# Kernel tuning notes

Hardware: AMD Instinct MI355X
Metric: run time of the kernel (lower is better)

The kernel has to match this reference:

```python
import jax, jax.numpy as jnp
import numpy as np

B, N, D = 8, 2352, 512          # N = SENT_LEN*(SENT_LEN+1) pair-grid layout
SENT_LEN, L, P = 48, 2, 512     # L = entity span length, P = number of relation pairs
NER_LABELS, RE_LABELS = 16, 32


def setup_inputs() -> dict:
    key = jax.random.key(0)
    ks = jax.random.split(key, 17)
    s = 0.02
    return {
        "inputs": jax.random.normal(ks[0], (B, N, D), jnp.float32),
        "ner": jax.random.normal(ks[1], (B, SENT_LEN, D), jnp.float32),
        "re_feat": jax.random.normal(ks[2], (P, D), jnp.float32),
        "adj": jax.random.uniform(ks[3], (B, N, N), jnp.float32),
        "W0_w": jax.random.normal(ks[4], (D, D), jnp.float32) * s,
        "W0_b": jnp.zeros((D,), jnp.float32),
        "W1_w": jax.random.normal(ks[5], (D, D), jnp.float32) * s,
        "W1_b": jnp.zeros((D,), jnp.float32),
        "out_w": jax.random.normal(ks[6], (2 * D, D), jnp.float32) * s,
        "out_b": jnp.zeros((D,), jnp.float32),
        "ner_w": jax.random.normal(ks[7], (2 * D, NER_LABELS), jnp.float32) * s,
        "ner_b": jnp.zeros((NER_LABELS,), jnp.float32),
        "re_w": jax.random.normal(ks[8], (2 * D, RE_LABELS), jnp.float32) * s,
        "re_b": jnp.zeros((RE_LABELS,), jnp.float32),
        "pair_sent": jax.random.randint(ks[9], (P,), 0, B),
        "head_start": jax.random.randint(ks[10], (P,), 0, SENT_LEN - L + 1),
        "tail_start": jax.random.randint(ks[11], (P,), 0, SENT_LEN - L + 1),
        "sent_len": SENT_LEN,
    }


def reference(inputs, ner, re_feat, adj, W0_w, W0_b, W1_w, W1_b, out_w, out_b,
              ner_w, ner_b, re_w, re_b, pair_sent, head_start, tail_start, sent_len):
    # --- GCN (use_rnn=False, dropout = identity / eval) ---
    denom = jnp.sum(adj, axis=2, keepdims=True) + 1.0      # [B, N, 1]
    x = inputs
    outs = []
    for Ww, Wb in ((W0_w, W0_b), (W1_w, W1_b)):
        Ax = jnp.einsum('bnm,bmd->bnd', adj, x)            # adj.bmm(x)
        AxW = (Ax @ Ww + Wb) + (x @ Ww + Wb)               # W(Ax) + W(x)
        g = jax.nn.relu(AxW / denom)
        outs.append(g)
        x = g
    logits = jnp.concatenate(outs, axis=-1) @ out_w + out_b  # [B, N, D]

    # --- NER head: first sent_len tokens per sentence (uniform lengths) ---
    ner_logits = jnp.concatenate([ner, logits[:, :sent_len]], axis=-1) @ ner_w + ner_b

    # --- RE head: ragged gather + average over (head span x tail span) grid ---
    offs = jnp.arange(L)
    i = head_start[:, None] + offs                         # [P, L]
    j = tail_start[:, None] + offs                         # [P, L]
    idx = (i[:, :, None] + 1) * sent_len + j[:, None, :]   # [P, L, L], get_re(l, i, j)
    pg = logits[pair_sent[:, None, None], idx]             # [P, L, L, D]
    avg = jnp.mean(pg, axis=(1, 2))                        # [P, D]
    re_logits = jnp.concatenate([re_feat, avg], axis=-1) @ re_w + re_b
    return ner_logits, re_logits
```

## Files before the change

### kernel.cpp

```cpp
#include <hip/hip_runtime.h>
#include <hip/hip_bf16.h>

#define B_    8
#define NP    2352
#define D_    512
#define SENT  48
#define PAIRS 512
#define NERL  16
#define REL   32
#define MTOT  (B_*NP)
#define SLOTB 640
#define MG    (B_*SLOTB)
#define GSCALE 32.0f

typedef unsigned short u16;
typedef unsigned char  u8;
typedef __bf16 bf16x8 __attribute__((ext_vector_type(8)));
typedef float  f32x4  __attribute__((ext_vector_type(4)));

__device__ __forceinline__ u16 f2b(float f) {
  union { float f; unsigned u; } c; c.f = f;
  unsigned u = c.u;
  u += 0x7fffu + ((u >> 16) & 1u);
  return (u16)(u >> 16);
}
__device__ __forceinline__ float b2f(u16 h) {
  union { unsigned u; float f; } c; c.u = ((unsigned)h) << 16;
  return c.f;
}
__device__ __forceinline__ u8 f2f8(float f) {
  unsigned u = __float_as_uint(f);
  u8 s = (u >> 24) & 0x80;
  float a = fabsf(f);
  if (a < 0.0009765625f) return s;
  if (a >= 448.f) return s | 0x7E;
  int e = ((u >> 23) & 0xFF) - 127;
  if (e < -6) {
    int q = (int)(a * 512.f + 0.5f);
    if (q >= 8) return s | 0x08;
    return s | (u8)q;
  }
  float sc = __uint_as_float((unsigned)((127 - e) << 23));
  int q = (int)(a * sc * 8.f + 0.5f);
  if (q >= 16) { q = 8; ++e; if (e > 8) return s | 0x7E; }
  return s | (u8)(((e + 7) << 3) | (q - 8));
}
#if defined(__has_builtin)
#if __has_builtin(__builtin_amdgcn_cvt_pk_fp8_f32)
#define HAVE_CVT_FP8 1
#endif
#endif
__device__ __forceinline__ unsigned f2f8x4(float a, float b, float c, float d) {
#ifdef HAVE_CVT_FP8
  unsigned w = 0;
  w = __builtin_amdgcn_cvt_pk_fp8_f32(a, b, w, false);
  w = __builtin_amdgcn_cvt_pk_fp8_f32(c, d, w, true);
  return w;
#else
  return (unsigned)f2f8(a) | ((unsigned)f2f8(b) << 8) |
         ((unsigned)f2f8(c) << 16) | ((unsigned)f2f8(d) << 24);
#endif
}
__device__ __forceinline__ float f82f(u8 v) {
  unsigned s = ((unsigned)(v & 0x80u)) << 24;
  unsigned e = (v >> 3) & 0xF, m = v & 7;
  if (e == 0) {
    if (m == 0) return __uint_as_float(s);
    float f = (float)m * 0.001953125f;
    return __uint_as_float(s | __float_as_uint(f));
  }
  return __uint_as_float(s | ((e + 120u) << 23) | (m << 20));
}
__device__ __forceinline__ void gload16(const void* g, void* lds) {
  __builtin_amdgcn_global_load_lds(
      (const __attribute__((address_space(1))) unsigned*)g,
      (__attribute__((address_space(3))) unsigned*)lds, 16, 0, 0);
}

template<int OUT8>
__device__ __forceinline__ void tcvt_body(const float* __restrict__ in_,
                                          void* __restrict__ out,
                                          int R, int C, int b, int r0, int c0,
                                          size_t inb, size_t outb,
                                          u16 tile[64][65]) {
  const int t  = threadIdx.x;
  const int tr = t >> 4, tc = (t & 15) * 4;
  #pragma unroll
  for (int i = 0; i < 4; ++i) {
    int rl = i * 16 + tr;
    int r  = r0 + rl;
    if (r < R) {
      const float* in = in_ + (size_t)b * inb + (size_t)r * C + c0 + tc;
      float4 v = *(const float4*)in;
      tile[rl][tc + 0] = f2b(v.x); tile[rl][tc + 1] = f2b(v.y);
      tile[rl][tc + 2] = f2b(v.z); tile[rl][tc + 3] = f2b(v.w);
    }
  }
  __syncthreads();
  const int c  = t >> 2;
  const int rb = (t & 3) * 16;
  #pragma unroll
  for (int i = 0; i < 4; ++i) {
    int rl = rb + i * 4;
    int r  = r0 + rl;
    if (OUT8) {
      u8* orow = (u8*)out + (size_t)b * outb + (size_t)(c0 + c) * R + r0;
      if (r + 3 < R) {
        *(unsigned*)(orow + rl) =
            f2f8x4(b2f(tile[rl + 0][c]), b2f(tile[rl + 1][c]),
                   b2f(tile[rl + 2][c]), b2f(tile[rl + 3][c]));
      } else {
        for (int j = 0; j < 4; ++j)
          if (r + j < R) orow[rl + j] = f2f8(b2f(tile[rl + j][c]));
      }
    } else {
      u16* orow = (u16*)out + (size_t)b * outb + (size_t)(c0 + c) * R + r0;
      if (r + 3 < R) {
        ushort4 v;
        v.x = tile[rl + 0][c]; v.y = tile[rl + 1][c];
        v.z = tile[rl + 2][c]; v.w = tile[rl + 3][c];
        *(ushort4*)(orow + rl) = v;
      } else {
        for (int j = 0; j < 4; ++j)
          if (r + j < R) orow[rl + j] = tile[rl + j][c];
      }
    }
  }
}

__global__ __launch_bounds__(256) void fat_prep(
    const float* __restrict__ adj, const float* __restrict__ inputs,
    const float* __restrict__ W0w, const float* __restrict__ W1w,
    const float* __restrict__ outw,
    const int* __restrict__ ps, const int* __restrict__ hs,
    const int* __restrict__ ts,
    u8* __restrict__ adj8, float* __restrict__ rdenom,
    u8* __restrict__ xt8, u16* __restrict__ w0t, u16* __restrict__ w1t,
    u16* __restrict__ owt, int* __restrict__ rowmap, int* __restrict__ pslot,
    u16* __restrict__ zp) {
  __shared__ u16 tile[64][65];
  __shared__ int sps[PAIRS];
  __shared__ float red[4];
  const int bx = blockIdx.x;
  const int t  = threadIdx.x;

  if (bx < MTOT) {
    const int row = bx;
    const float4* src = (const float4*)(adj + (size_t)row * NP);
    u8* dst = adj8 + (size_t)row * NP;
    float s = 0.f;
    for (int i = t; i < NP / 4; i += 256) {
      float4 v = src[i];
      s += (v.x + v.y) + (v.z + v.w);
      *(unsigned*)(dst + i * 4) = f2f8x4(v.x, v.y, v.z, v.w);
    }
    #pragma unroll
    for (int o = 32; o > 0; o >>= 1) s += __shfl_down(s, o, 64);
    int w = t >> 6, l = t & 63;
    if (l == 0) red[w] = s;
    __syncthreads();
    if (t == 0)
      rdenom[row] = 1.f / (red[0] + red[1] + red[2] + red[3] + 1.f);
  } else if (bx == MTOT) {
    zp[t] = 0; zp[256 + t] = 0;
  } else if (bx == MTOT + 1) {
    sps[t] = ps[t]; sps[256 + t] = ps[256 + t];
    for (int i = t; i < MG; i += 256) rowmap[i] = 0;
    __syncthreads();
    for (int u = t; u < B_ * SENT; u += 256)
      rowmap[(u / SENT) * SLOTB + (u % SENT)] = u % SENT;
    for (int p = t; p < PAIRS; p += 256) {
      const int b = sps[p];
      int rank = 0;
      for (int q = 0; q < p; ++q) rank += (sps[q] == b) ? 1 : 0;
      const int h = hs[p], tt = ts[p];
      const int s0 = b * SLOTB + SENT + 4 * rank;
      rowmap[s0 + 0] = (h + 1) * SENT + tt;
      rowmap[s0 + 1] = (h + 1) * SENT + tt + 1;
      rowmap[s0 + 2] = (h + 2) * SENT + tt;
      rowmap[s0 + 3] = (h + 2) * SENT + tt + 1;
      pslot[p] = s0;
    }
  } else {
    int r = bx - (MTOT + 2);
    if (r < 2368) {
      const int b = r / 296, rem = r % 296;
      const int rx = rem % 37, ry = rem / 37;
      tcvt_body<1>(inputs, xt8, NP, D_, b, rx * 64, ry * 64,
                   (size_t)NP * D_, (size_t)D_ * NP, tile);
    } else if ((r -= 2368) < 64) {
      tcvt_body<0>(W0w, w0t, 512, 512, 0, (r % 8) * 64, (r / 8) * 64,
                   0, 0, tile);
    } else if ((r -= 64) < 64) {
      tcvt_body<0>(W1w, w1t, 512, 512, 0, (r % 8) * 64, (r / 8) * 64,
                   0, 0, tile);
    } else {
      r -= 64;
      tcvt_body<0>(outw, owt, 1024, 512, 0, (r % 16) * 64, (r / 16) * 64,
                   0, 0, tile);
    }
  }
}

template<int MODE, int WRITE_T, int GATHER>
__global__ __launch_bounds__(256, 2) void gemm8(
    const void* __restrict__ A, const void* __restrict__ A2,
    const void* __restrict__ Bm, const u16* __restrict__ Xt,
    const float* __restrict__ bias, const float* __restrict__ rdenom,
    const int* __restrict__ rowmap,
    const u16* __restrict__ zp, u16* __restrict__ out, u8* __restrict__ outT,
    float ascale)
{
  constexpr bool F8   = (MODE == 0);
  constexpr int KACT   = (MODE == 0) ? NP : (MODE == 1 ? 512 : 1024);
  constexpr int KTILES = (KACT + 63) / 64;
  constexpr int EPC    = F8 ? 16 : 8;
  constexpr int CPT    = F8 ? 4 : 8;
  constexpr int NJ     = F8 ? 2 : 4;
  constexpr int ABYTES = F8 ? 8192 : 16384;

  int m0, n0, bat = 0;
  const u8* Ab = (const u8*)A;
  const u8* Bb = (const u8*)Bm;
  size_t outBase = 0;
  if constexpr (GATHER) {
    const int bx  = blockIdx.x;
    const int rid = (bx & 7) * 20 + (bx >> 3);
    const int mt  = rid >> 2;
    n0 = (rid & 3) << 7;
    m0 = mt * 128;
    bat = mt / 5;
    if constexpr (MODE == 0) {
      Ab = (const u8*)A  + (size_t)bat * NP * NP;
      Bb = (const u8*)Bm + (size_t)bat * 512 * NP;
    }
  } else if constexpr (MODE == 0) {
    const int bx  = blockIdx.x;
    bat = bx & 7;
    const int loc = bx >> 3;
    const int mt  = loc >> 2;
    n0 = (loc & 3) << 7;
    m0 = (mt < 18) ? mt * 128 : NP - 128;
    Ab = (const u8*)A  + (size_t)bat * NP * NP;
    Bb = (const u8*)Bm + (size_t)bat * 512 * NP;
    outBase = (size_t)bat * NP * 512;
  } else {
    const int bx  = blockIdx.x;
    const int xcd = bx & 7, pos = bx >> 3;
    const int rid = (xcd < 4) ? xcd * 74 + pos : 296 + (xcd - 4) * 73 + pos;
    const int mt  = rid >> 2;
    n0 = (rid & 3) << 7;
    m0 = mt * 128;
  }

  __shared__ __align__(16) u8 As[2 * ABYTES];
  __shared__ __align__(16) u8 Bs[2 * ABYTES];

  const int tid = threadIdx.x;
  const int l  = tid & 63;
  const int w  = tid >> 6;
  const int wm = w >> 1, wn = w & 1;
  const int lr = l & 15, lq = l >> 4;

  f32x4 acc[4][4];
  #pragma unroll
  for (int i = 0; i < 4; ++i)
    #pragma unroll
    for (int j = 0; j < 4; ++j)
      acc[i][j] = (f32x4){0.f, 0.f, 0.f, 0.f};

  int rsrc[2];
  #pragma unroll
  for (int j = 0; j < 2; ++j) {
    const int row = j * 64 + (tid >> 2);
    if constexpr (GATHER && MODE != 1) rsrc[j] = rowmap[m0 + row];
    else                               rsrc[j] = m0 + row;
  }

  auto STAGE = [&](int isA, int d, int kt) {
    #pragma unroll
    for (int j = 0; j < NJ; ++j) {
      const int cl   = j * 256 + tid;
      const int row  = (cl >> 2) & 127;
      const int slot = cl & 3;
      const int s    = F8 ? 0 : (cl >> 9);
      const int gch  = kt * CPT + s * 4 + (slot ^ ((row >> 1) & 3));
      const u8* src;
      if (isA) {
        if constexpr (MODE == 0) {
          src = Ab + (size_t)rsrc[j & 1] * NP + (size_t)gch * 16;
        } else if constexpr (MODE == 1) {
          src = (const u8*)A + ((size_t)(m0 + row) * 512 + (size_t)gch * 8) * 2;
        } else {
          int rg = (GATHER ? rsrc[j & 1] : (m0 + row));
          src = (gch < 64)
              ? (const u8*)A  + (((size_t)(GATHER ? bat * NP : 0) + rg) * 512
                                 + (size_t)gch * 8) * 2
              : (const u8*)A2 + ((size_t)(m0 + row) * 512
                                 + (size_t)(gch - 64) * 8) * 2;
        }
        if (gch * EPC + EPC > KACT) src = (const u8*)zp;
        gload16(src, As + d * ABYTES + cl * 16);
      } else {
        if constexpr (F8)
          src = Bb + (size_t)(n0 + row) * NP + (size_t)gch * 16;
        else
          src = (const u8*)Bm + ((size_t)(n0 + row) * KACT + (size_t)gch * 8) * 2;
        if (gch * EPC + EPC > KACT) src = (const u8*)zp;
        gload16(src, Bs + d * ABYTES + cl * 16);
      }
    }
  };

  STAGE(1, 0, 0);
  STAGE(0, 0, 0);
  asm volatile("s_waitcnt vmcnt(0)" ::: "memory");
  __builtin_amdgcn_s_barrier();

  int d = 0;
  for (int kt = 0; kt < KTILES; ++kt) {
    if (kt + 1 < KTILES) {
      STAGE(1, d ^ 1, kt + 1);
      STAGE(0, d ^ 1, kt + 1);
    }
    const u8* Ad = As + d * ABYTES;
    const u8* Bd = Bs + d * ABYTES;
    if constexpr (F8) {
      long a0[4], b0[4], a1[4], b1[4];
      #pragma unroll
      for (int f = 0; f < 4; ++f) {
        const int ra = wm * 64 + f * 16 + lr;
        const int rb = wn * 64 + f * 16 + lr;
        const int swa = (ra >> 1) & 3, swb = (rb >> 1) & 3;
        const int co = (lq >> 1), bo = (lq & 1) << 3;
        a0[f] = *(const long*)(Ad + ra * 64 + (((0 + co) ^ swa) << 4) + bo);
        b0[f] = *(const long*)(Bd + rb * 64 + (((0 + co) ^ swb) << 4) + bo);
        a1[f] = *(const long*)(Ad + ra * 64 + (((2 + co) ^ swa) << 4) + bo);
        b1[f] = *(const long*)(Bd + rb * 64 + (((2 + co) ^ swb) << 4) + bo);
      }
      asm volatile("s_waitcnt lgkmcnt(0)" ::: "memory");
      __builtin_amdgcn_sched_barrier(0);
      __builtin_amdgcn_s_setprio(1);
      #pragma unroll
      for (int mf = 0; mf < 4; ++mf)
        #pragma unroll
        for (int nf = 0; nf < 4; ++nf)
          acc[mf][nf] = __builtin_amdgcn_mfma_f32_16x16x32_fp8_fp8(
              a0[mf], b0[nf], acc[mf][nf], 0, 0, 0);
      #pragma unroll
      for (int mf = 0; mf < 4; ++mf)
        #pragma unroll
        for (int nf = 0; nf < 4; ++nf)
          acc[mf][nf] = __builtin_amdgcn_mfma_f32_16x16x32_fp8_fp8(
              a1[mf], b1[nf], acc[mf][nf], 0, 0, 0);
      __builtin_amdgcn_s_setprio(0);
      __builtin_amdgcn_sched_barrier(0);
    } else {
      bf16x8 a0[4], b0[4], a1[4], b1[4];
      #pragma unroll
      for (int f = 0; f < 4; ++f) {
        const int ra = wm * 64 + f * 16 + lr;
        const int rb = wn * 64 + f * 16 + lr;
        const int sa = (lq ^ ((ra >> 1) & 3)) << 4;
        const int sb = (lq ^ ((rb >> 1) & 3)) << 4;
        a0[f] = *(const bf16x8*)(Ad + ra * 64 + sa);
        b0[f] = *(const bf16x8*)(Bd + rb * 64 + sb);
        a1[f] = *(const bf16x8*)(Ad + 8192 + ra * 64 + sa);
        b1[f] = *(const bf16x8*)(Bd + 8192 + rb * 64 + sb);
      }
      asm volatile("s_waitcnt lgkmcnt(0)" ::: "memory");
      __builtin_amdgcn_sched_barrier(0);
      __builtin_amdgcn_s_setprio(1);
      #pragma unroll
      for (int mf = 0; mf < 4; ++mf)
        #pragma unroll
        for (int nf = 0; nf < 4; ++nf)
          acc[mf][nf] = __builtin_amdgcn_mfma_f32_16x16x32_bf16(
              a0[mf], b0[nf], acc[mf][nf], 0, 0, 0);
      #pragma unroll
      for (int mf = 0; mf < 4; ++mf)
        #pragma unroll
        for (int nf = 0; nf < 4; ++nf)
          acc[mf][nf] = __builtin_amdgcn_mfma_f32_16x16x32_bf16(
              a1[mf], b1[nf], acc[mf][nf], 0, 0, 0);
      __builtin_amdgcn_s_setprio(0);
      __builtin_amdgcn_sched_barrier(0);
    }
    asm volatile("s_waitcnt vmcnt(0)" ::: "memory");
    __builtin_amdgcn_s_barrier();
    d ^= 1;
  }

  #pragma unroll
  for (int mf = 0; mf < 4; ++mf) {
    const int gm0 = m0 + wm * 64 + mf * 16 + lq * 4;
    f32x4 rd;
    if constexpr (MODE == 1) {
      if constexpr (GATHER) {
        #pragma unroll
        for (int r = 0; r < 4; ++r)
          rd[r] = rdenom[(size_t)bat * NP + rowmap[gm0 + r]];
      } else {
        rd = *(const f32x4*)(rdenom + gm0);
      }
    }
    int rsm[4];
    if constexpr (GATHER && MODE == 0) {
      #pragma unroll
      for (int r = 0; r < 4; ++r) rsm[r] = rowmap[gm0 + r];
    }
    #pragma unroll
    for (int nf = 0; nf < 4; ++nf) {
      const int gn = n0 + wn * 64 + nf * 16 + lr;
      float vf[4];
      if constexpr (MODE == 0) {
        float xf[4];
        if constexpr (GATHER) {
          #pragma unroll
          for (int r = 0; r < 4; ++r)
            xf[r] = b2f(Xt[((size_t)bat * NP + rsm[r]) * 512 + gn]);
        } else {
          uchar4 xv = *(const uchar4*)(Bb + (size_t)gn * NP + gm0);
          xf[0] = f82f(xv.x); xf[1] = f82f(xv.y);
          xf[2] = f82f(xv.z); xf[3] = f82f(xv.w);
        }
        #pragma unroll
        for (int r = 0; r < 4; ++r) vf[r] = acc[mf][nf][r] * ascale + xf[r];
      } else if constexpr (MODE == 1) {
        const float bn = 2.f * bias[gn];
        #pragma unroll
        for (int r = 0; r < 4; ++r)
          vf[r] = fmaxf((acc[mf][nf][r] + bn) * rd[r], 0.f);
      } else {
        const float bn = bias[gn];
        #pragma unroll
        for (int r = 0; r < 4; ++r) vf[r] = acc[mf][nf][r] + bn;
      }
      #pragma unroll
      for (int r = 0; r < 4; ++r)
        out[outBase + (size_t)(gm0 + r) * 512 + gn] = f2b(vf[r]);
      if constexpr (WRITE_T) {
        const int bb = gm0 / NP;
        const int ml = gm0 - bb * NP;
        *(unsigned*)(outT + ((size_t)bb * 512 + gn) * NP + ml) =
            f2f8x4(vf[0] * GSCALE, vf[1] * GSCALE,
                   vf[2] * GSCALE, vf[3] * GSCALE);
      }
    }
  }
}

__global__ __launch_bounds__(256) void heads_kernel(
    const float* __restrict__ ner, const u16* __restrict__ logits_g,
    const float* __restrict__ nw, const float* __restrict__ nb,
    const float* __restrict__ refeat, const float* __restrict__ rw,
    const float* __restrict__ rb, const int* __restrict__ pslot,
    float* __restrict__ outp) {
  __shared__ float avg[D_];
  if (blockIdx.x < 96) {
    const int r = blockIdx.x * 4 + (threadIdx.x >> 6);
    const int b = r / SENT, tp = r % SENT;
    const int lane = threadIdx.x & 63;
    const float* nrow = ner      + ((size_t)b * SENT  + tp) * D_;
    const u16*   lrow = logits_g + ((size_t)b * SLOTB + tp) * D_;
    float rv[16];
    #pragma unroll
    for (int i = 0; i < 8; ++i) rv[i]     = nrow[lane + i * 64];
    #pragma unroll
    for (int i = 0; i < 8; ++i) rv[8 + i] = b2f(lrow[lane + i * 64]);
    for (int j = 0; j < NERL; ++j) {
      float s = 0.f;
      #pragma unroll
      for (int i = 0; i < 16; ++i)
        s = fmaf(rv[i], nw[(size_t)(lane + i * 64) * NERL + j], s);
      for (int o = 32; o > 0; o >>= 1) s += __shfl_down(s, o);
      if (lane == 0) outp[r * NERL + j] = s + nb[j];
    }
  } else {
    const int p = blockIdx.x - 96;
    const u16* r0 = logits_g + (size_t)pslot[p] * D_;
    for (int dd = threadIdx.x; dd < D_; dd += 256)
      avg[dd] = 0.25f * (b2f(r0[dd]) + b2f(r0[D_ + dd]) +
                         b2f(r0[2 * D_ + dd]) + b2f(r0[3 * D_ + dd]));
    __syncthreads();
    const int wave = threadIdx.x >> 6, lane = threadIdx.x & 63;
    const float* rf = refeat + (size_t)p * D_;
    float* out = outp + B_ * SENT * NERL;
    for (int jj = 0; jj < 8; ++jj) {
      int j = wave * 8 + jj;
      float s = 0.f;
      #pragma unroll
      for (int i = 0; i < 8; ++i) {
        int k = lane + i * 64;
        s = fmaf(rf[k],  rw[(size_t)k * REL + j], s);
        s = fmaf(avg[k], rw[(size_t)(k + D_) * REL + j], s);
      }
      for (int o = 32; o > 0; o >>= 1) s += __shfl_down(s, o);
      if (lane == 0) out[p * REL + j] = s + rb[j];
    }
  }
}

extern "C" void kernel_launch(void* const* d_in, const int* in_sizes, int n_in,
                              void* d_out, int out_size, void* d_ws, size_t ws_size,
                              hipStream_t stream) {
  const float* inputs = (const float*)d_in[0];
  const float* ner    = (const float*)d_in[1];
  const float* refeat = (const float*)d_in[2];
  const float* adj    = (const float*)d_in[3];
  const float* W0w    = (const float*)d_in[4];
  const float* W0b    = (const float*)d_in[5];
  const float* W1w    = (const float*)d_in[6];
  const float* W1b    = (const float*)d_in[7];
  const float* outw   = (const float*)d_in[8];
  const float* outb   = (const float*)d_in[9];
  const float* nerw   = (const float*)d_in[10];
  const float* nerb   = (const float*)d_in[11];
  const float* rew    = (const float*)d_in[12];
  const float* reb    = (const float*)d_in[13];
  const int*   ps     = (const int*)d_in[14];
  const int*   hs     = (const int*)d_in[15];
  const int*   ts     = (const int*)d_in[16];
  (void)in_sizes; (void)n_in; (void)out_size; (void)ws_size;
  float* outp = (float*)d_out;

  char* ws = (char*)d_ws;
  size_t off = 0;
  u8* adj8 = (u8*)(ws + off); off += (size_t)B_ * NP * NP;
  float* rdenom = (float*)(ws + off); off += (size_t)MTOT * 4;
  u16* zp  = (u16*)(ws + off); off += 1024;
  u16* w0t = (u16*)(ws + off); off += 512 * 512 * 2;
  u16* w1t = (u16*)(ws + off); off += 512 * 512 * 2;
  u16* owt = (u16*)(ws + off); off += 512 * 1024 * 2;
  u8*  xt8 = (u8*)(ws + off); off += (size_t)B_ * 512 * NP;
  u16* S   = (u16*)(ws + off); off += (size_t)MTOT * 512 * 2;
  u16* g0  = (u16*)(ws + off); off += (size_t)MTOT * 512 * 2;
  int* rowmap = (int*)(ws + off); off += (size_t)MG * 4;
  int* pslot  = (int*)(ws + off); off += (size_t)PAIRS * 4;
  u16* S_g      = (u16*)(ws + off); off += (size_t)MG * 512 * 2;
  u16* g1_g     = (u16*)(ws + off); off += (size_t)MG * 512 * 2;
  u16* logits_g = (u16*)(ws + off); off += (size_t)MG * 512 * 2;

  const int FATG = MTOT + 2 + 2368 + 64 + 64 + 128;
  fat_prep<<<FATG, 256, 0, stream>>>(adj, inputs, W0w, W1w, outw, ps, hs, ts,
                                     adj8, rdenom, xt8, w0t, w1t, owt,
                                     rowmap, pslot, zp);

  gemm8<0,0,0><<<608, 256, 0, stream>>>(adj8, nullptr, xt8, nullptr,
                                        nullptr, nullptr, nullptr, zp, S,
                                        nullptr, 1.0f);
  gemm8<1,1,0><<<588, 256, 0, stream>>>(S, nullptr, w0t, nullptr,
                                        W0b, rdenom, nullptr, zp, g0,
                                        xt8, 1.0f);
  gemm8<0,0,1><<<160, 256, 0, stream>>>(adj8, nullptr, xt8, g0,
                                        nullptr, nullptr, rowmap, zp, S_g,
                                        nullptr, 1.0f / GSCALE);
  gemm8<1,0,1><<<160, 256, 0, stream>>>(S_g, nullptr, w1t, nullptr,
                                        W1b, rdenom, rowmap, zp, g1_g,
                                        nullptr, 1.0f);
  gemm8<2,0,1><<<160, 256, 0, stream>>>(g0, g1_g, owt, nullptr,
                                        outb, nullptr, rowmap, zp, logits_g,
                                        nullptr, 1.0f);

  heads_kernel<<<608, 256, 0, stream>>>(ner, logits_g, nerw, nerb,
                                        refeat, rew, reb, pslot, outp);
}
```

Before: 284.5 us.

## Fuse adjacency fp8 conversion and row-sum into the first GEMM's A loader

This drops the separate prep pass that turned fp32 adj into an fp8 copy and computed the reciprocal degree. Both GEMMs that read adj now load the fp32 tiles into registers, convert them to fp8 and write them to LDS. The non-gather adj GEMM also accumulates row sums and writes rdenom from its n0==0 blocks. The aim is to remove the write and re-read of the 44MB fp8 adj copy and one kernel's worth of traffic. In exchange, each adj row is re-read in fp32 by four N-tile blocks, and the A path no longer uses async direct-to-LDS loads, so load latency is hidden less well.

```diff
diff --git a/kernel.cpp b/kernel.cpp
--- a/kernel.cpp
+++ b/kernel.cpp
@@ -129,41 +129,22 @@
 }
 
 __global__ __launch_bounds__(256) void fat_prep(
-    const float* __restrict__ adj, const float* __restrict__ inputs,
+    const float* __restrict__ inputs,
     const float* __restrict__ W0w, const float* __restrict__ W1w,
     const float* __restrict__ outw,
     const int* __restrict__ ps, const int* __restrict__ hs,
     const int* __restrict__ ts,
-    u8* __restrict__ adj8, float* __restrict__ rdenom,
     u8* __restrict__ xt8, u16* __restrict__ w0t, u16* __restrict__ w1t,
     u16* __restrict__ owt, int* __restrict__ rowmap, int* __restrict__ pslot,
     u16* __restrict__ zp) {
   __shared__ u16 tile[64][65];
   __shared__ int sps[PAIRS];
-  __shared__ float red[4];
   const int bx = blockIdx.x;
   const int t  = threadIdx.x;
 
-  if (bx < MTOT) {
-    const int row = bx;
-    const float4* src = (const float4*)(adj + (size_t)row * NP);
-    u8* dst = adj8 + (size_t)row * NP;
-    float s = 0.f;
-    for (int i = t; i < NP / 4; i += 256) {
-      float4 v = src[i];
-      s += (v.x + v.y) + (v.z + v.w);
-      *(unsigned*)(dst + i * 4) = f2f8x4(v.x, v.y, v.z, v.w);
-    }
-    #pragma unroll
-    for (int o = 32; o > 0; o >>= 1) s += __shfl_down(s, o, 64);
-    int w = t >> 6, l = t & 63;
-    if (l == 0) red[w] = s;
-    __syncthreads();
-    if (t == 0)
-      rdenom[row] = 1.f / (red[0] + red[1] + red[2] + red[3] + 1.f);
-  } else if (bx == MTOT) {
+  if (bx == 0) {
     zp[t] = 0; zp[256 + t] = 0;
-  } else if (bx == MTOT + 1) {
+  } else if (bx == 1) {
     sps[t] = ps[t]; sps[256 + t] = ps[256 + t];
     for (int i = t; i < MG; i += 256) rowmap[i] = 0;
     __syncthreads();
@@ -182,7 +163,7 @@
       pslot[p] = s0;
     }
   } else {
-    int r = bx - (MTOT + 2);
+    int r = bx - 2;
     if (r < 2368) {
       const int b = r / 296, rem = r % 296;
       const int rx = rem % 37, ry = rem / 37;
@@ -206,7 +187,7 @@
 __global__ __launch_bounds__(256, 2) void gemm8(
     const void* __restrict__ A, const void* __restrict__ A2,
     const void* __restrict__ Bm, const u16* __restrict__ Xt,
-    const float* __restrict__ bias, const float* __restrict__ rdenom,
+    const float* __restrict__ bias, float* __restrict__ rdenom,
     const int* __restrict__ rowmap,
     const u16* __restrict__ zp, u16* __restrict__ out, u8* __restrict__ outT,
     float ascale)
@@ -216,13 +197,13 @@
   constexpr int KTILES = (KACT + 63) / 64;
   constexpr int EPC    = F8 ? 16 : 8;
   constexpr int CPT    = F8 ? 4 : 8;
-  constexpr int NJ     = F8 ? 2 : 4;
   constexpr int ABYTES = F8 ? 8192 : 16384;
 
   int m0, n0, bat = 0;
-  const u8* Ab = (const u8*)A;
+  const float* Af = (const float*)A;
   const u8* Bb = (const u8*)Bm;
   size_t outBase = 0;
+  bool ovl = false;
   if constexpr (GATHER) {
     const int bx  = blockIdx.x;
     const int rid = (bx & 7) * 20 + (bx >> 3);
@@ -231,7 +212,7 @@
     m0 = mt * 128;
     bat = mt / 5;
     if constexpr (MODE == 0) {
-      Ab = (const u8*)A  + (size_t)bat * NP * NP;
+      Af = (const float*)A + (size_t)bat * NP * NP;
       Bb = (const u8*)Bm + (size_t)bat * 512 * NP;
     }
   } else if constexpr (MODE == 0) {
@@ -241,7 +222,8 @@
     const int mt  = loc >> 2;
     n0 = (loc & 3) << 7;
     m0 = (mt < 18) ? mt * 128 : NP - 128;
-    Ab = (const u8*)A  + (size_t)bat * NP * NP;
+    ovl = (mt == 18);
+    Af = (const float*)A + (size_t)bat * NP * NP;
     Bb = (const u8*)Bm + (size_t)bat * 512 * NP;
     outBase = (size_t)bat * NP * 512;
   } else {
@@ -277,51 +259,102 @@
     else                               rsrc[j] = m0 + row;
   }
 
-  auto STAGE = [&](int isA, int d, int kt) {
-    #pragma unroll
-    for (int j = 0; j < NJ; ++j) {
+  float4 ar[8];
+  float rsum0 = 0.f, rsum1 = 0.f;
+  auto A_LOAD = [&](int kt) {
+    #pragma unroll
+    for (int j = 0; j < 2; ++j) {
       const int cl   = j * 256 + tid;
       const int row  = (cl >> 2) & 127;
       const int slot = cl & 3;
-      const int s    = F8 ? 0 : (cl >> 9);
-      const int gch  = kt * CPT + s * 4 + (slot ^ ((row >> 1) & 3));
+      const int gch  = kt * 4 + (slot ^ ((row >> 1) & 3));
+      const float* src = Af + (size_t)rsrc[j] * NP + gch * 16;
+      if (gch * 16 + 16 > NP) src = (const float*)zp;
+      #pragma unroll
+      for (int q = 0; q < 4; ++q) ar[j * 4 + q] = *(const float4*)(src + q * 4);
+    }
+  };
+  auto A_WRITE = [&](int d) {
+    #pragma unroll
+    for (int j = 0; j < 2; ++j) {
+      const int cl = j * 256 + tid;
+      uint4 pk;
+      pk.x = f2f8x4(ar[j*4+0].x, ar[j*4+0].y, ar[j*4+0].z, ar[j*4+0].w);
+      pk.y = f2f8x4(ar[j*4+1].x, ar[j*4+1].y, ar[j*4+1].z, ar[j*4+1].w);
+      pk.z = f2f8x4(ar[j*4+2].x, ar[j*4+2].y, ar[j*4+2].z, ar[j*4+2].w);
+      pk.w = f2f8x4(ar[j*4+3].x, ar[j*4+3].y, ar[j*4+3].z, ar[j*4+3].w);
+      *(uint4*)(As + d * ABYTES + cl * 16) = pk;
+      if constexpr (MODE == 0 && !GATHER) {
+        float s = (ar[j*4+0].x + ar[j*4+0].y) + (ar[j*4+0].z + ar[j*4+0].w)
+                + (ar[j*4+1].x + ar[j*4+1].y) + (ar[j*4+1].z + ar[j*4+1].w)
+                + (ar[j*4+2].x + ar[j*4+2].y) + (ar[j*4+2].z + ar[j*4+2].w)
+                + (ar[j*4+3].x + ar[j*4+3].y) + (ar[j*4+3].z + ar[j*4+3].w);
+        if (j == 0) rsum0 += s; else rsum1 += s;
+      }
+    }
+  };
+  auto STAGE_B = [&](int d, int kt) {
+    #pragma unroll
+    for (int j = 0; j < 2; ++j) {
+      const int cl   = j * 256 + tid;
+      const int row  = (cl >> 2) & 127;
+      const int slot = cl & 3;
+      const int gch  = kt * 4 + (slot ^ ((row >> 1) & 3));
+      const u8* src  = Bb + (size_t)(n0 + row) * NP + (size_t)gch * 16;
+      if (gch * 16 + 16 > KACT) src = (const u8*)zp;
+      gload16(src, Bs + d * ABYTES + cl * 16);
+    }
+  };
+  auto STAGE_BF16 = [&](int isA, int d, int kt) {
+    #pragma unroll
+    for (int j = 0; j < 4; ++j) {
+      const int cl   = j * 256 + tid;
+      const int row  = (cl >> 2) & 127;
+      const int slot = cl & 3;
+      const int s    = cl >> 9;
+      const int gch  = kt * 8 + s * 4 + (slot ^ ((row >> 1) & 3));
       const u8* src;
       if (isA) {
-        if constexpr (MODE == 0) {
-          src = Ab + (size_t)rsrc[j & 1] * NP + (size_t)gch * 16;
-        } else if constexpr (MODE == 1) {
-          src = (const u8*)A + ((size_t)(m0 + row) * 512 + (size_t)gch * 8) * 2;
-        } else {
+        if constexpr (MODE == 2) {
           int rg = (GATHER ? rsrc[j & 1] : (m0 + row));
           src = (gch < 64)
               ? (const u8*)A  + (((size_t)(GATHER ? bat * NP : 0) + rg) * 512
                                  + (size_t)gch * 8) * 2
               : (const u8*)A2 + ((size_t)(m0 + row) * 512
                                  + (size_t)(gch - 64) * 8) * 2;
+        } else {
+          src = (const u8*)A + ((size_t)(m0 + row) * 512 + (size_t)gch * 8) * 2;
         }
         if (gch * EPC + EPC > KACT) src = (const u8*)zp;
         gload16(src, As + d * ABYTES + cl * 16);
       } else {
-        if constexpr (F8)
-          src = Bb + (size_t)(n0 + row) * NP + (size_t)gch * 16;
-        else
-          src = (const u8*)Bm + ((size_t)(n0 + row) * KACT + (size_t)gch * 8) * 2;
+        src = (const u8*)Bm + ((size_t)(n0 + row) * KACT + (size_t)gch * 8) * 2;
         if (gch * EPC + EPC > KACT) src = (const u8*)zp;
         gload16(src, Bs + d * ABYTES + cl * 16);
       }
     }
   };
 
-  STAGE(1, 0, 0);
-  STAGE(0, 0, 0);
-  asm volatile("s_waitcnt vmcnt(0)" ::: "memory");
+  if constexpr (F8) {
+    A_LOAD(0);
+    STAGE_B(0, 0);
+    asm volatile("s_waitcnt vmcnt(0)" ::: "memory");
+    A_WRITE(0);
+    asm volatile("s_waitcnt lgkmcnt(0)" ::: "memory");
+  } else {
+    STAGE_BF16(1, 0, 0);
+    STAGE_BF16(0, 0, 0);
+    asm volatile("s_waitcnt vmcnt(0)" ::: "memory");
+  }
   __builtin_amdgcn_s_barrier();
 
   int d = 0;
   for (int kt = 0; kt < KTILES; ++kt) {
-    if (kt + 1 < KTILES) {
-      STAGE(1, d ^ 1, kt + 1);
-      STAGE(0, d ^ 1, kt + 1);
+    const bool more = (kt + 1 < KTILES);
+    if constexpr (F8) {
+      if (more) { A_LOAD(kt + 1); STAGE_B(d ^ 1, kt + 1); }
+    } else {
+      if (more) { STAGE_BF16(1, d ^ 1, kt + 1); STAGE_BF16(0, d ^ 1, kt + 1); }
     }
     const u8* Ad = As + d * ABYTES;
     const u8* Bd = Bs + d * ABYTES;
@@ -355,6 +388,11 @@
               a1[mf], b1[nf], acc[mf][nf], 0, 0, 0);
       __builtin_amdgcn_s_setprio(0);
       __builtin_amdgcn_sched_barrier(0);
+      asm volatile("s_waitcnt vmcnt(0)" ::: "memory");
+      if (more) {
+        A_WRITE(d ^ 1);
+        asm volatile("s_waitcnt lgkmcnt(0)" ::: "memory");
+      }
     } else {
       bf16x8 a0[4], b0[4], a1[4], b1[4];
       #pragma unroll
@@ -385,10 +423,24 @@
               a1[mf], b1[nf], acc[mf][nf], 0, 0, 0);
       __builtin_amdgcn_s_setprio(0);
       __builtin_amdgcn_sched_barrier(0);
-    }
-    asm volatile("s_waitcnt vmcnt(0)" ::: "memory");
+      asm volatile("s_waitcnt vmcnt(0)" ::: "memory");
+    }
     __builtin_amdgcn_s_barrier();
     d ^= 1;
+  }
+
+  if constexpr (MODE == 0 && !GATHER) {
+    if (n0 == 0) {
+      #pragma unroll
+      for (int j = 0; j < 2; ++j) {
+        float s = (j == 0) ? rsum0 : rsum1;
+        s += __shfl_xor(s, 1, 64);
+        s += __shfl_xor(s, 2, 64);
+        const int lrow = j * 64 + (tid >> 2);
+        if ((l & 3) == 0 && (!ovl || m0 + lrow >= 2304))
+          rdenom[(size_t)bat * NP + m0 + lrow] = 1.f / (s + 1.f);
+      }
+    }
   }
 
   #pragma unroll
@@ -526,7 +578,6 @@
 
   char* ws = (char*)d_ws;
   size_t off = 0;
-  u8* adj8 = (u8*)(ws + off); off += (size_t)B_ * NP * NP;
   float* rdenom = (float*)(ws + off); off += (size_t)MTOT * 4;
   u16* zp  = (u16*)(ws + off); off += 1024;
   u16* w0t = (u16*)(ws + off); off += 512 * 512 * 2;
@@ -541,25 +592,24 @@
   u16* g1_g     = (u16*)(ws + off); off += (size_t)MG * 512 * 2;
   u16* logits_g = (u16*)(ws + off); off += (size_t)MG * 512 * 2;
 
-  const int FATG = MTOT + 2 + 2368 + 64 + 64 + 128;
-  fat_prep<<<FATG, 256, 0, stream>>>(adj, inputs, W0w, W1w, outw, ps, hs, ts,
-                                     adj8, rdenom, xt8, w0t, w1t, owt,
-                                     rowmap, pslot, zp);
-
-  gemm8<0,0,0><<<608, 256, 0, stream>>>(adj8, nullptr, xt8, nullptr,
-                                        nullptr, nullptr, nullptr, zp, S,
+  const int FATG = 2 + 2368 + 64 + 64 + 128;
+  fat_prep<<<FATG, 256, 0, stream>>>(inputs, W0w, W1w, outw, ps, hs, ts,
+                                     xt8, w0t, w1t, owt, rowmap, pslot, zp);
+
+  gemm8<0,0,0><<<608, 256, 0, stream>>>(adj, nullptr, xt8, nullptr,
+                                        nullptr, rdenom, nullptr, zp, S,
                                         nullptr, 1.0f);
   gemm8<1,1,0><<<588, 256, 0, stream>>>(S, nullptr, w0t, nullptr,
                                         W0b, rdenom, nullptr, zp, g0,
                                         xt8, 1.0f);
-  gemm8<0,0,1><<<160, 256, 0, stream>>>(adj8, nullptr, xt8, g0,
-                                        nullptr, nullptr, rowmap, zp, S_g,
+  gemm8<0,0,1><<<160, 256, 0, stream>>>(adj, nullptr, xt8, g0,
+                                        nullptr, rdenom, rowmap, zp, S_g,
                                         nullptr, 1.0f / GSCALE);
   gemm8<1,0,1><<<160, 256, 0, stream>>>(S_g, nullptr, w1t, nullptr,
                                         W1b, rdenom, rowmap, zp, g1_g,
                                         nullptr, 1.0f);
   gemm8<2,0,1><<<160, 256, 0, stream>>>(g0, g1_g, owt, nullptr,
-                                        outb, nullptr, rowmap, zp, logits_g,
+                                        outb, rdenom, rowmap, zp, logits_g,
                                         nullptr, 1.0f);
 
   heads_kernel<<<608, 256, 0, stream>>>(ner, logits_g, nerw, nerb,
```

New measurement: 370.5 us. +30.2%, slower.
